# Kernel optimization log

Hardware: AMD Instinct MI355X
Metric: run time of the kernel (lower is better)

Reference implementation:

```python
import jax, jax.numpy as jnp
import numpy as np

NEG = -1e30  # safe -inf surrogate (avoids nan grads through where)
NUM_CLASSES = 128
BLANK = NUM_CLASSES - 1
B, T, L = 256, 512, 64


def setup_inputs() -> dict:
    key = jax.random.key(0)
    k1, k2, k3, k4 = jax.random.split(key, 4)
    y_pred = jax.random.normal(k1, (B, T, NUM_CLASSES), dtype=jnp.float32)
    y_true = jax.random.randint(k2, (B, L), 0, BLANK, dtype=jnp.int32)  # labels in [0, C-2]
    input_length = jax.random.randint(k3, (B,), T // 2, T + 1, dtype=jnp.int32)
    label_length = jax.random.randint(k4, (B,), L // 2, L + 1, dtype=jnp.int32)
    return {"y_true": y_true, "y_pred": y_pred,
            "input_length": input_length, "label_length": label_length}


def ctc_loss(y_pred, y_true, input_length, label_length):
    # y_pred: [B,T,C] logits (batch-major), y_true: [B,L] int labels, blank = C-1.
    Bs, Ts, C = y_pred.shape
    Ls = y_true.shape[1]
    S = 2 * Ls + 1  # extended label lattice: blank, l1, blank, l2, ..., blank
    lp = jax.nn.log_softmax(y_pred.astype(jnp.float32), axis=-1)  # [B,T,C]
    z = jnp.full((Bs, S), BLANK, dtype=jnp.int32).at[:, 1::2].set(y_true)  # [B,S]
    idx = jnp.broadcast_to(z[:, None, :], (Bs, Ts, S))
    lp_z = jnp.take_along_axis(lp, idx, axis=2)  # [B,T,S] log p(z_s | t)
    # skip transition s-2 -> s allowed when z_s is a label differing from z_{s-2}
    s_idx = jnp.arange(S)
    z_m2 = jnp.pad(z[:, :-2], ((0, 0), (2, 0)), constant_values=BLANK)
    skip = (s_idx[None, :] >= 2) & (z != BLANK) & (z != z_m2)  # [B,S]
    alpha0 = (jnp.full((Bs, S), NEG, jnp.float32)
              .at[:, 0].set(lp_z[:, 0, 0])
              .at[:, 1].set(lp_z[:, 0, 1]))
    lps = jnp.moveaxis(lp_z[:, 1:, :], 1, 0)  # [T-1, B, S]
    ts = jnp.arange(1, Ts)

    def step(alpha, xs):
        t, lpt = xs
        a1 = jnp.pad(alpha[:, :-1], ((0, 0), (1, 0)), constant_values=NEG)
        a2 = jnp.where(skip, jnp.pad(alpha[:, :-2], ((0, 0), (2, 0)), constant_values=NEG), NEG)
        new = jnp.logaddexp(jnp.logaddexp(alpha, a1), a2) + lpt
        # freeze rows whose sequence already ended (t >= input_length)
        alpha = jnp.where((t < input_length)[:, None], new, alpha)
        return alpha, None

    alphaT, _ = jax.lax.scan(step, alpha0, (ts, lps))
    e1 = (2 * label_length)[:, None]  # final blank position per row
    a_end = jnp.take_along_axis(alphaT, e1, axis=1)[:, 0]
    a_end2 = jnp.take_along_axis(alphaT, e1 - 1, axis=1)[:, 0]
    return -jnp.logaddexp(a_end, a_end2)  # [B] negative log-likelihood


def reference(y_true, y_pred, input_length, label_length):
    # tf.nn.ctc_loss(labels, logits, label_length, logit_length,
    #                logits_time_major=False, blank_index=num_classes-1)
    return ctc_loss(y_pred, y_true, input_length, label_length)
```

## Files before the change

### kernel.cpp

```cpp
#include <hip/hip_runtime.h>
#include <hip/hip_fp16.h>
#include <math.h>


constexpr int Cc = 128;
constexpr int Tt = 512;
constexpr int Ll = 64;
constexpr float INV_LN2 = 1.4426950408889634f;
constexpr float LN2_F   = 0.6931471805599453f;

__device__ __forceinline__ float fexp2(float x) { return __builtin_amdgcn_exp2f(x); }
__device__ __forceinline__ float flog2(float x) { return __builtin_amdgcn_logf(x); }

template<int CTRL, bool BC>
__device__ __forceinline__ float dppf(float old, float x) {
    return __int_as_float(__builtin_amdgcn_update_dpp(
        __float_as_int(old), __float_as_int(x), CTRL, 0xF, 0xF, BC));
}
__device__ __forceinline__ float wshr1(float x, float fill) { return dppf<0x138, false>(fill, x); }

__device__ __forceinline__ float rlf(float v, int lane) {
    return __int_as_float(__builtin_amdgcn_readlane(__float_as_int(v), lane));
}
__device__ __forceinline__ float rowsum(float e) {
    e += dppf<0x111, true>(0.f, e);
    e += dppf<0x112, true>(0.f, e);
    e += dppf<0x114, true>(0.f, e);
    e += dppf<0x118, true>(0.f, e);
    return e;
}
__device__ __forceinline__ float rowmax(float m) {
    m = fmaxf(m, dppf<0x111, true>(0.f, m));
    m = fmaxf(m, dppf<0x112, true>(0.f, m));
    m = fmaxf(m, dppf<0x114, true>(0.f, m));
    m = fmaxf(m, dppf<0x118, true>(0.f, m));
    return m;
}
__device__ __forceinline__ float allmax(float m) {
    m = rowmax(m);
    return fmaxf(fmaxf(rlf(m, 15), rlf(m, 31)), fmaxf(rlf(m, 47), rlf(m, 63)));
}
__device__ __forceinline__ float bperm_f(int srclane, float v) {
    return __int_as_float(__builtin_amdgcn_ds_bpermute(srclane << 2, __float_as_int(v)));
}
__device__ __forceinline__ float gather4(float4 v, int srclane, int csel) {
    const float gx = bperm_f(srclane, v.x), gy = bperm_f(srclane, v.y);
    const float gz = bperm_f(srclane, v.z), gw = bperm_f(srclane, v.w);
    const float lo = (csel & 1) ? gy : gx;
    const float hi = (csel & 1) ? gw : gz;
    return (csel & 2) ? hi : lo;
}

template<bool GUARD>
__device__ __forceinline__ void do_chunk(uint4 raw, int t0, int inlen, float skf,
                                         float& aO, float& aE, float& r0, float& Rtot)
{
    float dv[8];
    {
        const __half2 h0 = *reinterpret_cast<const __half2*>(&raw.x);
        const __half2 h1 = *reinterpret_cast<const __half2*>(&raw.y);
        const __half2 h2 = *reinterpret_cast<const __half2*>(&raw.z);
        const __half2 h3 = *reinterpret_cast<const __half2*>(&raw.w);
        dv[0] = __low2float(h0); dv[1] = __high2float(h0);
        dv[2] = __low2float(h1); dv[3] = __high2float(h1);
        dv[4] = __low2float(h2); dv[5] = __high2float(h2);
        dv[6] = __low2float(h3); dv[7] = __high2float(h3);
    }
#pragma unroll
    for (int j = 0; j < 8; ++j) {
        if (!GUARD || (t0 + j < inlen)) {
            const float pE = wshr1(aE, r0);
            const float pO = wshr1(aO, 0.0f);
            const float nO = (fmaf(skf, pO, pE) + aO) * dv[j];
            aE += aO;
            aO = nO;
        }
    }
    const float M_ = allmax(fmaxf(fmaxf(aO, aE), r0));
    int R_ = (int)(__float_as_uint(M_) >> 23) - 127;
    R_ = (R_ < 0) ? 0 : ((R_ > 126) ? 126 : R_);
    const float sc = __uint_as_float((unsigned)(127 - R_) << 23);
    aO = fminf(aO * sc, 4.0f);
    aE = fminf(aE * sc, 4.0f);
    r0 = fminf(r0 * sc, 4.0f);
    Rtot += (float)R_;
}

__global__ __launch_bounds__(1024, 1) void ctc_fused2_kernel(
    const int* __restrict__ y_true,
    const float* __restrict__ y_pred,
    const int* __restrict__ in_len,
    const int* __restrict__ lab_len,
    float* __restrict__ out)
{
    __shared__ __half w_lds[Tt / 8][64][8];
    __shared__ float  ps[16];

    const int b   = blockIdx.x;
    const int tid = threadIdx.x;
    const int w   = tid >> 6;
    const int l   = tid & 63;

    int inlen = in_len[b]; if (inlen < 1) inlen = 1; if (inlen > Tt) inlen = Tt;
    int LLv   = lab_len[b]; if (LLv < 1) LLv = 1; if (LLv > Ll) LLv = Ll;

    const int lab = y_true[b * Ll + l] & 127;
    const float* rowbase = y_pred + (size_t)b * Tt * Cc;

    const int half = l >> 5, li = l & 31;
    const int srcA = lab >> 2;
    const int csel = lab & 3;
    const int tbase = w * 32;
    const bool live = (l < LLv);

    float4 vb[4];
#pragma unroll
    for (int j = 0; j < 4; ++j)
        vb[j] = ((const float4*)(rowbase + (size_t)(tbase + 2 * j + half) * Cc))[li];

    float acc = 0.0f;

    for (int i = 0; i < 16; i += 4) {
#pragma unroll
        for (int j = 0; j < 4; ++j) {
            const float4 v = vb[j];
            const int nx = i + 4 + j;
            if (nx < 16)
                vb[j] = ((const float4*)(rowbase + (size_t)(tbase + 2 * nx + half) * Cc))[li];

            const int rA = tbase + 2 * (i + j);
            const int rB = rA + 1;

            float e = (fexp2(v.x * INV_LN2) + fexp2(v.y * INV_LN2))
                    + (fexp2(v.z * INV_LN2) + fexp2(v.w * INV_LN2));
            e = rowsum(e);
            const float sA = rlf(e, 15) + rlf(e, 31);
            const float sB = rlf(e, 47) + rlf(e, 63);
            const float lsA = flog2(sA), lsB = flog2(sB);
            const float blA = rlf(v.w, 31);
            const float blB = rlf(v.w, 63);

            const float lpbA = fmaf(blA, INV_LN2, -lsA);
            const float lpbB = fmaf(blB, INV_LN2, -lsB);
            acc += ((rA < inlen) ? lpbA : 0.0f) + ((rB < inlen) ? lpbB : 0.0f);

            const float xA = gather4(v, srcA, csel);
            const float xB = gather4(v, srcA + 32, csel);
            float wA = fminf(fmaxf(fexp2((xA - blA) * INV_LN2), 6.1e-5f), 8192.0f);
            float wB = fminf(fmaxf(fexp2((xB - blB) * INV_LN2), 6.1e-5f), 8192.0f);
            wA = live ? wA : 0.0f;
            wB = live ? wB : 0.0f;
            const unsigned packed =
                  (unsigned)__half_as_ushort(__float2half(wA))
                | ((unsigned)__half_as_ushort(__float2half(wB)) << 16);
            *(unsigned*)&w_lds[rA >> 3][l][rA & 7] = packed;
        }
    }
    if (l == 0) ps[w] = acc;

    __syncthreads();
    if (w != 0) return;

    const int labp = __shfl_up(lab, 1, 64);
    const float skf = ((l >= 1) && (lab != labp)) ? 1.0f : 0.0f;

    float aO = 0.0f, aE = 0.0f, r0 = 1.0f, Rtot = 0.0f;

    const int nchunks = (inlen + 7) >> 3;
    uint4 A = *(const uint4*)&w_lds[0][l][0];
    for (int c = 0; c < nchunks; ++c) {
        const int nx = (c + 1 < Tt / 8) ? c + 1 : Tt / 8 - 1;
        const uint4 Bv = *(const uint4*)&w_lds[nx][l][0];
        const int t0 = c * 8;
        if (t0 + 8 <= inlen) do_chunk<false>(A, t0, inlen, skf, aO, aE, r0, Rtot);
        else                 do_chunk<true >(A, t0, inlen, skf, aO, aE, r0, Rtot);
        A = Bv;
    }

    float cum_b = 0.0f;
#pragma unroll
    for (int q = 0; q < 16; ++q) cum_b += ps[q];

    const float aEr = __shfl(aE, LLv - 1, 64);
    const float aOr = __shfl(aO, LLv - 1, 64);
    if (l == 0)
        out[b] = -LN2_F * (flog2(fmaxf(aEr + aOr, 1e-37f)) + Rtot + cum_b);
}

extern "C" void kernel_launch(void* const* d_in, const int* in_sizes, int n_in,
                              void* d_out, int out_size, void* d_ws, size_t ws_size,
                              hipStream_t stream) {
    const int*   y_true  = (const int*)d_in[0];
    const float* y_pred  = (const float*)d_in[1];
    const int*   in_len  = (const int*)d_in[2];
    const int*   lab_len = (const int*)d_in[3];
    float*       out     = (float*)d_out;
    (void)d_ws; (void)ws_size;

    ctc_fused2_kernel<<<256, 1024, 0, stream>>>(y_true, y_pred, in_len, lab_len, out);
}
```

Measured before the change: 118.3 us.

## Overlap producer waves with the alpha recursion using LDS round counters

Wave 0 becomes a dedicated consumer that runs the CTC recursion. The other 15 waves produce the per-chunk label weights round-robin and signal each finished round through LDS atomic counters, so the block-wide barrier goes away. Wave 0 spin-waits with s_sleep on those counters and can start the serial recursion while later chunks are still being computed. The inner step is also rewritten as chained FMAs with a precomputed skip*weight product. The risks are one fewer producer wave, polling overhead, and relying on volatile LDS reads plus waitcnt to order the data correctly.

```diff
diff --git a/kernel.cpp b/kernel.cpp
--- a/kernel.cpp
+++ b/kernel.cpp
@@ -6,6 +6,9 @@
 constexpr int Cc = 128;
 constexpr int Tt = 512;
 constexpr int Ll = 64;
+constexpr int NCH = Tt / 8;
+constexpr int NPW = 15;
+constexpr int NR  = (NCH + NPW - 1) / NPW;
 constexpr float INV_LN2 = 1.4426950408889634f;
 constexpr float LN2_F   = 0.6931471805599453f;
 
@@ -66,12 +69,16 @@
         dv[4] = __low2float(h2); dv[5] = __high2float(h2);
         dv[6] = __low2float(h3); dv[7] = __high2float(h3);
     }
+    float sd[8];
+#pragma unroll
+    for (int j = 0; j < 8; ++j) sd[j] = skf * dv[j];
 #pragma unroll
     for (int j = 0; j < 8; ++j) {
         if (!GUARD || (t0 + j < inlen)) {
+            const float ad = aO * dv[j];
             const float pE = wshr1(aE, r0);
             const float pO = wshr1(aO, 0.0f);
-            const float nO = (fmaf(skf, pO, pE) + aO) * dv[j];
+            const float nO = fmaf(pE, dv[j], fmaf(pO, sd[j], ad));
             aE += aO;
             aO = nO;
         }
@@ -86,100 +93,130 @@
     Rtot += (float)R_;
 }
 
-__global__ __launch_bounds__(1024, 1) void ctc_fused2_kernel(
+__global__ __launch_bounds__(1024, 1) void ctc_fused3_kernel(
     const int* __restrict__ y_true,
     const float* __restrict__ y_pred,
     const int* __restrict__ in_len,
     const int* __restrict__ lab_len,
     float* __restrict__ out)
 {
-    __shared__ __half w_lds[Tt / 8][64][8];
-    __shared__ float  ps[16];
+    __shared__ __half w_lds[NCH][64][8];
+    __shared__ float  ps[NPW];
+    __shared__ int    rctr[NR];
 
     const int b   = blockIdx.x;
     const int tid = threadIdx.x;
     const int w   = tid >> 6;
     const int l   = tid & 63;
 
+    if (tid < NR) rctr[tid] = 0;
+    __syncthreads();
+
     int inlen = in_len[b]; if (inlen < 1) inlen = 1; if (inlen > Tt) inlen = Tt;
     int LLv   = lab_len[b]; if (LLv < 1) LLv = 1; if (LLv > Ll) LLv = Ll;
 
     const int lab = y_true[b * Ll + l] & 127;
     const float* rowbase = y_pred + (size_t)b * Tt * Cc;
 
-    const int half = l >> 5, li = l & 31;
-    const int srcA = lab >> 2;
-    const int csel = lab & 3;
-    const int tbase = w * 32;
-    const bool live = (l < LLv);
-
-    float4 vb[4];
-#pragma unroll
-    for (int j = 0; j < 4; ++j)
-        vb[j] = ((const float4*)(rowbase + (size_t)(tbase + 2 * j + half) * Cc))[li];
-
-    float acc = 0.0f;
-
-    for (int i = 0; i < 16; i += 4) {
-#pragma unroll
-        for (int j = 0; j < 4; ++j) {
-            const float4 v = vb[j];
-            const int nx = i + 4 + j;
-            if (nx < 16)
-                vb[j] = ((const float4*)(rowbase + (size_t)(tbase + 2 * nx + half) * Cc))[li];
-
-            const int rA = tbase + 2 * (i + j);
-            const int rB = rA + 1;
-
-            float e = (fexp2(v.x * INV_LN2) + fexp2(v.y * INV_LN2))
-                    + (fexp2(v.z * INV_LN2) + fexp2(v.w * INV_LN2));
-            e = rowsum(e);
-            const float sA = rlf(e, 15) + rlf(e, 31);
-            const float sB = rlf(e, 47) + rlf(e, 63);
-            const float lsA = flog2(sA), lsB = flog2(sB);
-            const float blA = rlf(v.w, 31);
-            const float blB = rlf(v.w, 63);
-
-            const float lpbA = fmaf(blA, INV_LN2, -lsA);
-            const float lpbB = fmaf(blB, INV_LN2, -lsB);
-            acc += ((rA < inlen) ? lpbA : 0.0f) + ((rB < inlen) ? lpbB : 0.0f);
-
-            const float xA = gather4(v, srcA, csel);
-            const float xB = gather4(v, srcA + 32, csel);
-            float wA = fminf(fmaxf(fexp2((xA - blA) * INV_LN2), 6.1e-5f), 8192.0f);
-            float wB = fminf(fmaxf(fexp2((xB - blB) * INV_LN2), 6.1e-5f), 8192.0f);
-            wA = live ? wA : 0.0f;
-            wB = live ? wB : 0.0f;
-            const unsigned packed =
-                  (unsigned)__half_as_ushort(__float2half(wA))
-                | ((unsigned)__half_as_ushort(__float2half(wB)) << 16);
-            *(unsigned*)&w_lds[rA >> 3][l][rA & 7] = packed;
-        }
-    }
-    if (l == 0) ps[w] = acc;
-
-    __syncthreads();
-    if (w != 0) return;
+    if (w != 0) {
+        const int pw   = w - 1;
+        const int half = l >> 5, li = l & 31;
+        const int srcA = lab >> 2;
+        const int csel = lab & 3;
+        const bool live = (l < LLv);
+
+        float acc = 0.0f;
+
+        float4 vb[4];
+#pragma unroll
+        for (int j = 0; j < 4; ++j)
+            vb[j] = ((const float4*)(rowbase + (size_t)(pw * 8 + 2 * j + half) * Cc))[li];
+
+        for (int c = pw, r = 0; c < NCH; c += NPW, ++r) {
+            const int cn = c + NPW;
+#pragma unroll
+            for (int j = 0; j < 4; ++j) {
+                const float4 v = vb[j];
+                if (cn < NCH)
+                    vb[j] = ((const float4*)(rowbase + (size_t)(cn * 8 + 2 * j + half) * Cc))[li];
+
+                const int rA = c * 8 + 2 * j;
+                const int rB = rA + 1;
+
+                float e = (fexp2(v.x * INV_LN2) + fexp2(v.y * INV_LN2))
+                        + (fexp2(v.z * INV_LN2) + fexp2(v.w * INV_LN2));
+                e = rowsum(e);
+                const float sA = rlf(e, 15) + rlf(e, 31);
+                const float sB = rlf(e, 47) + rlf(e, 63);
+                const float lsA = flog2(sA), lsB = flog2(sB);
+                const float blA = rlf(v.w, 31);
+                const float blB = rlf(v.w, 63);
+
+                const float lpbA = fmaf(blA, INV_LN2, -lsA);
+                const float lpbB = fmaf(blB, INV_LN2, -lsB);
+                acc += ((rA < inlen) ? lpbA : 0.0f) + ((rB < inlen) ? lpbB : 0.0f);
+
+                const float xA = gather4(v, srcA, csel);
+                const float xB = gather4(v, srcA + 32, csel);
+                float wA = fminf(fmaxf(fexp2((xA - blA) * INV_LN2), 6.1e-5f), 8192.0f);
+                float wB = fminf(fmaxf(fexp2((xB - blB) * INV_LN2), 6.1e-5f), 8192.0f);
+                wA = live ? wA : 0.0f;
+                wB = live ? wB : 0.0f;
+                const unsigned packed =
+                      (unsigned)__half_as_ushort(__float2half(wA))
+                    | ((unsigned)__half_as_ushort(__float2half(wB)) << 16);
+                *(unsigned*)&w_lds[c][l][2 * j] = packed;
+            }
+            if (cn >= NCH && l == 0) ps[pw] = acc;
+            asm volatile("s_waitcnt lgkmcnt(0)" ::: "memory");
+            if (l == 0) atomicAdd(&rctr[r], 1);
+        }
+        return;
+    }
 
     const int labp = __shfl_up(lab, 1, 64);
     const float skf = ((l >= 1) && (lab != labp)) ? 1.0f : 0.0f;
 
     float aO = 0.0f, aE = 0.0f, r0 = 1.0f, Rtot = 0.0f;
-
     const int nchunks = (inlen + 7) >> 3;
+
+    volatile int* vctr = rctr;
+    int ready = 0, rr = 0;
+    auto wait_upto = [&](int cneed) {
+        while (ready <= cneed) {
+            const int rem  = NCH - rr * NPW;
+            const int need = rem < NPW ? rem : NPW;
+            if (vctr[rr] >= need) { ready += need; ++rr; }
+            else __builtin_amdgcn_s_sleep(1);
+        }
+        asm volatile("" ::: "memory");
+    };
+
+    wait_upto(0);
     uint4 A = *(const uint4*)&w_lds[0][l][0];
     for (int c = 0; c < nchunks; ++c) {
-        const int nx = (c + 1 < Tt / 8) ? c + 1 : Tt / 8 - 1;
-        const uint4 Bv = *(const uint4*)&w_lds[nx][l][0];
+        uint4 Bv = A;
+        if (c + 1 < nchunks) {
+            wait_upto(c + 1);
+            Bv = *(const uint4*)&w_lds[c + 1][l][0];
+        }
         const int t0 = c * 8;
         if (t0 + 8 <= inlen) do_chunk<false>(A, t0, inlen, skf, aO, aE, r0, Rtot);
         else                 do_chunk<true >(A, t0, inlen, skf, aO, aE, r0, Rtot);
         A = Bv;
     }
 
+    while (rr < NR) {
+        const int rem  = NCH - rr * NPW;
+        const int need = rem < NPW ? rem : NPW;
+        if (vctr[rr] >= need) ++rr;
+        else __builtin_amdgcn_s_sleep(1);
+    }
+    asm volatile("" ::: "memory");
+
     float cum_b = 0.0f;
 #pragma unroll
-    for (int q = 0; q < 16; ++q) cum_b += ps[q];
+    for (int q = 0; q < NPW; ++q) cum_b += ps[q];
 
     const float aEr = __shfl(aE, LLv - 1, 64);
     const float aOr = __shfl(aO, LLv - 1, 64);
@@ -197,5 +234,5 @@
     float*       out     = (float*)d_out;
     (void)d_ws; (void)ws_size;
 
-    ctc_fused2_kernel<<<256, 1024, 0, stream>>>(y_true, y_pred, in_len, lab_len, out);
-}
+    ctc_fused3_kernel<<<256, 1024, 0, stream>>>(y_true, y_pred, in_len, lab_len, out);
+}
```

After: 111.7 us. -5.6%, faster.
